# Performance work log

Hardware: AMD Instinct MI355X
Metric: run time of the kernel (lower is better)

Reference implementation:

```python
import jax, jax.numpy as jnp
import numpy as np
from jax import lax
import math

B, C, H, W = 8, 512, 24, 24
L = H * W
D_STATE = 16
D_INNER = 2 * C
DT_RANK = C // 16
K = 4
SCALE = 1.0 / math.sqrt(C)


def layer_norm(x, g, b, eps=1e-5):
    m = x.mean(-1, keepdims=True)
    v = ((x - m) ** 2).mean(-1, keepdims=True)
    return (x - m) * lax.rsqrt(v + eps) * g + b


def selective_scan(u, delta, A, Bm, Cm, Ds):
    # u, delta: (B,K,d,L); Bm, Cm: (B,K,N,L); A: (K,d,N); Ds: (K,d)
    us = jnp.moveaxis(u, -1, 0)      # (L,B,K,d)
    dts = jnp.moveaxis(delta, -1, 0)
    Bs = jnp.moveaxis(Bm, -1, 0)     # (L,B,K,N)
    Cs = jnp.moveaxis(Cm, -1, 0)

    def step(h, inp):
        u_t, dt_t, B_t, C_t = inp
        dA = jnp.exp(dt_t[..., None] * A)                      # (B,K,d,N)
        dBu = (dt_t * u_t)[..., None] * B_t[:, :, None, :]     # (B,K,d,N)
        h = dA * h + dBu
        y = jnp.einsum('bkdn,bkn->bkd', h, C_t)
        return h, y

    h0 = jnp.zeros(u.shape[:3] + (A.shape[-1],), u.dtype)
    _, ys = lax.scan(step, h0, (us, dts, Bs, Cs))
    y = jnp.moveaxis(ys, 0, -1)                                # (B,K,d,L)
    return y + Ds[None, :, :, None] * u


def ss2d(x, in_proj_w, dwconv_w, dwconv_b, x_proj_w, dt_proj_w, dt_proj_b,
         A_logs, Ds, out_norm_g, out_norm_b, out_proj_w):
    # x: (B,H,W,C) channel-last
    xz = x @ in_proj_w.T                                       # (B,H,W,2*d_inner)
    xi, z = jnp.split(xz, 2, axis=-1)
    xc = xi.transpose(0, 3, 1, 2)                              # (B,d_inner,H,W)
    xc = lax.conv_general_dilated(xc, dwconv_w, (1, 1), 'SAME',
                                  feature_group_count=D_INNER,
                                  dimension_numbers=('NCHW', 'OIHW', 'NCHW'))
    xc = jax.nn.silu(xc + dwconv_b[None, :, None, None])
    x_hw = xc.reshape(B, D_INNER, L)
    x_wh = xc.transpose(0, 1, 3, 2).reshape(B, D_INNER, L)
    xs = jnp.stack([x_hw, x_wh, x_hw[..., ::-1], x_wh[..., ::-1]], axis=1)  # (B,4,d,L)
    x_dbl = jnp.einsum('bkdl,kcd->bkcl', xs, x_proj_w)
    dt, Bm, Cm = jnp.split(x_dbl, [DT_RANK, DT_RANK + D_STATE], axis=2)
    delta = jax.nn.softplus(jnp.einsum('bkrl,kdr->bkdl', dt, dt_proj_w)
                            + dt_proj_b[None, :, :, None])
    A = -jnp.exp(A_logs)
    ys = selective_scan(xs, delta, A, Bm, Cm, Ds)              # (B,4,d,L)
    y_wh = ys[:, 1].reshape(B, D_INNER, W, H).transpose(0, 1, 3, 2).reshape(B, D_INNER, L)
    y_whr = ys[:, 3, :, ::-1].reshape(B, D_INNER, W, H).transpose(0, 1, 3, 2).reshape(B, D_INNER, L)
    y = ys[:, 0] + ys[:, 2, :, ::-1] + y_wh + y_whr
    y = y.reshape(B, D_INNER, H, W).transpose(0, 2, 3, 1)      # (B,H,W,d_inner)
    y = layer_norm(y, out_norm_g, out_norm_b)
    y = y * jax.nn.silu(z)
    return y @ out_proj_w.T                                    # (B,H,W,C)


def setup_inputs():
    key = jax.random.key(0)
    ks = jax.random.split(key, 10)
    n = lambda k, sh, s=0.02: jax.random.normal(k, sh, dtype=jnp.float32) * s
    return {
        'x5': jax.random.normal(ks[0], (B, C, H, W), dtype=jnp.float32),
        'conv_w': n(ks[1], (C, C)),
        'conv_b': jnp.zeros((C,), jnp.float32),
        'ln1_g': jnp.ones((C,), jnp.float32),
        'ln1_b': jnp.zeros((C,), jnp.float32),
        'in_proj_w': n(ks[2], (2 * D_INNER, C)),
        'dwconv_w': n(ks[3], (D_INNER, 1, 3, 3), 0.1),
        'dwconv_b': jnp.zeros((D_INNER,), jnp.float32),
        'x_proj_w': n(ks[4], (K, DT_RANK + 2 * D_STATE, D_INNER)),
        'dt_proj_w': n(ks[5], (K, D_INNER, DT_RANK), 0.1),
        'dt_proj_b': n(ks[6], (K, D_INNER), 0.1),
        'A_logs': jnp.tile(jnp.log(jnp.arange(1, D_STATE + 1, dtype=jnp.float32))[None, None, :],
                           (K, D_INNER, 1)),
        'Ds': jnp.ones((K, D_INNER), jnp.float32),
        'out_norm_g': jnp.ones((D_INNER,), jnp.float32),
        'out_norm_b': jnp.zeros((D_INNER,), jnp.float32),
        'out_proj_w': n(ks[7], (C, D_INNER)),
    }


def reference(x5, conv_w, conv_b, ln1_g, ln1_b, in_proj_w, dwconv_w, dwconv_b,
              x_proj_w, dt_proj_w, dt_proj_b, A_logs, Ds, out_norm_g, out_norm_b,
              out_proj_w):
    # 1x1 conv + residual
    x5 = jnp.einsum('bchw,oc->bohw', x5, conv_w) + conv_b[None, :, None, None] + x5
    x0 = x5.transpose(0, 2, 3, 1)                              # (B,H,W,C)
    # VSSBlock: x + SS2D(LN(x)); called twice on same input with same weights -> identical
    x00 = x0 + ss2d(layer_norm(x0, ln1_g, ln1_b), in_proj_w, dwconv_w, dwconv_b,
                    x_proj_w, dt_proj_w, dt_proj_b, A_logs, Ds,
                    out_norm_g, out_norm_b, out_proj_w)
    xq = x00.transpose(0, 3, 1, 2).reshape(B, C, L)            # (B,C,L)
    xq_flat = xq.transpose(0, 2, 1).reshape(B * L, C)          # (B*L, C)
    xk_flat = xq.transpose(1, 0, 2).reshape(C, B * L)          # (C, B*L)
    xw = (xq_flat @ xk_flat) * SCALE                           # (B*L, B*L)
    xw = xw.reshape(B * L, B, L).max(-1).mean(-1).reshape(B, L)
    xw = jax.nn.softmax(xw, axis=-1)
    norm0 = x5 / jnp.maximum(jnp.linalg.norm(x5, axis=1, keepdims=True), 1e-12)
    xw = xw[:, None, :]                                        # (B,1,L)
    xw_max = xw.max(-1, keepdims=True)
    mask = (xw == xw_max).astype(x5.dtype).reshape(B, 1, H, W)  # winner-take-all
    seeds = (norm0 * mask).sum((2, 3))                         # (B,C)
    # correlation (eval branch: relu), seeds act as 1x1 conv weights
    cor = jax.nn.relu(jnp.einsum('bchw,oc->bohw', norm0, seeds)).mean(1).reshape(B, L)
    mn = cor.min(1, keepdims=True)
    mx = cor.max(1, keepdims=True)
    cormap = ((cor - mn) / (mx - mn + 1e-12)).reshape(B, 1, H, W)
    x51 = x5 * cormap
    proto1 = x51.mean((0, 2, 3), keepdims=True)                # (1,C,1,1)
    return (x5, proto1, x5 * proto1 + x51, mask)
```

## Files before the change

kernel.cpp:

```cpp
#include <hip/hip_runtime.h>
#include <math.h>

#define NB 8
#define NC 512
#define NH 24
#define NW 24
#define NL 576
#define ND 1024
#define NBL 4608
#define NCH 8
#define CL 72

typedef __attribute__((ext_vector_type(8))) short bf16x8;
typedef __attribute__((ext_vector_type(4))) float f32x4;
typedef __attribute__((ext_vector_type(2))) float f32x2;

__device__ __forceinline__ unsigned enc_f(float f){
    unsigned u = __float_as_uint(f);
    return (u & 0x80000000u) ? ~u : (u | 0x80000000u);
}
__device__ __forceinline__ float dec_f(unsigned e){
    return (e & 0x80000000u) ? __uint_as_float(e ^ 0x80000000u) : __uint_as_float(~e);
}

__device__ __forceinline__ int scan_idx(int t, int k){
    int t2 = (k >= 2) ? (NL - 1 - t) : t;
    return (k & 1) ? ((t2 % NH) * NW + t2 / NH) : t2;
}

__device__ __forceinline__ float softplus_f(float x){
    return fmaxf(x, 0.f) + __logf(1.f + __expf(-fabsf(x)));
}
__device__ __forceinline__ float silu_f(float x){
    return x / (1.f + __expf(-x));
}

__device__ __forceinline__ void split_bf(float v, unsigned short &h, unsigned short &l){
    unsigned u = __float_as_uint(v);
    unsigned hr = (u + 0x7fffu + ((u>>16)&1u)) >> 16;
    h = (unsigned short)hr;
    float hf = __uint_as_float(hr << 16);
    unsigned u2 = __float_as_uint(v - hf);
    l = (unsigned short)((u2 + 0x7fffu + ((u2>>16)&1u)) >> 16);
}

__global__ void k_transpose_in(const float* __restrict__ x5, float* __restrict__ x5t,
                               unsigned short* __restrict__ x5tB){
    __shared__ float t[32][33];
    const int b = blockIdx.z;
    const int c0 = blockIdx.x*32, l0 = blockIdx.y*32;
    const int tx = threadIdx.x & 31, ty = threadIdx.x >> 5;
    #pragma unroll
    for (int i=ty; i<32; i+=8)
        t[i][tx] = x5[((size_t)b*NC + c0 + i)*NL + l0 + tx];
    __syncthreads();
    #pragma unroll
    for (int i=ty; i<32; i+=8){
        float v = t[tx][i];
        x5t[((size_t)b*NL + l0 + i)*NC + c0 + tx] = v;
        unsigned short hh, ll; split_bf(v, hh, ll);
        size_t rb = ((size_t)b*NL + l0 + i)*1536 + c0 + tx;
        x5tB[rb] = hh; x5tB[rb+512] = ll; x5tB[rb+1024] = hh;
    }
}

template<int FORM>
__global__ void k_split(const float* __restrict__ in, unsigned short* __restrict__ oA,
                        unsigned short* __restrict__ oB, int K, int total4){
    int t = blockIdx.x*256 + threadIdx.x;
    if (t >= total4) return;
    int kq = K >> 2;
    int r = t / kq; int k4 = (t - r*kq) << 2;
    float4 v = *(const float4*)(in + (size_t)r*K + k4);
    float vv[4] = {v.x, v.y, v.z, v.w};
    unsigned short h[4], lo[4];
    #pragma unroll
    for (int i=0;i<4;i++) split_bf(vv[i], h[i], lo[i]);
    unsigned hp0 = h[0] | ((unsigned)h[1]<<16), hp1 = h[2] | ((unsigned)h[3]<<16);
    unsigned lp0 = lo[0] | ((unsigned)lo[1]<<16), lp1 = lo[2] | ((unsigned)lo[3]<<16);
    size_t base = (size_t)r*3*K + k4;
    if (FORM == 0 || FORM == 2){
        unsigned* p0 = (unsigned*)(oA + base);
        unsigned* p1 = (unsigned*)(oA + base + K);
        unsigned* p2 = (unsigned*)(oA + base + 2*K);
        p0[0]=hp0; p0[1]=hp1;  p1[0]=hp0; p1[1]=hp1;  p2[0]=lp0; p2[1]=lp1;
    }
    if (FORM == 1 || FORM == 2){
        unsigned short* o = (FORM==2) ? oB : oA;
        unsigned* p0 = (unsigned*)(o + base);
        unsigned* p1 = (unsigned*)(o + base + K);
        unsigned* p2 = (unsigned*)(o + base + 2*K);
        p0[0]=hp0; p0[1]=hp1;  p1[0]=lp0; p1[1]=lp1;  p2[0]=hp0; p2[1]=hp1;
    }
}

template<int MODE>
__launch_bounds__(256)
__global__ void mfma_nt(const unsigned short* __restrict__ A, const unsigned short* __restrict__ Bm,
                        const float* __restrict__ R0, const float* __restrict__ R1,
                        float* __restrict__ out0, float* __restrict__ out1,
                        unsigned* __restrict__ mbuf, int K3)
{
    int bi, bj;
    if (MODE == 4){
        int rem = blockIdx.x, len = 36; bi = 0;
        while (rem >= len){ rem -= len; len--; bi++; }
        bj = bi + rem;
    } else { bi = blockIdx.x; bj = blockIdx.y; }
    const int m0 = bi*128, n0 = bj*128;
    __shared__ __align__(16) unsigned short As[128*32];
    __shared__ __align__(16) unsigned short Bs[128*32];
    const int tid = threadIdx.x;
    const int w = tid >> 6, l = tid & 63;
    const int mw = (w>>1)*64, nw = (w&1)*64;
    const int fr = l & 15, fq = l >> 4;

    f32x4 acc[4][4];
    #pragma unroll
    for (int i=0;i<4;i++)
        #pragma unroll
        for (int j=0;j<4;j++)
            #pragma unroll
            for (int c=0;c<4;c++) acc[i][j][c] = 0.f;

    const int c0 = tid, c1 = tid + 256;
    const int r0 = c0 >> 2, o0 = (c0 & 3) * 8;
    const int r1 = c1 >> 2, o1 = (c1 & 3) * 8;
    const unsigned short* pA0 = A  + (size_t)(m0 + r0)*K3 + o0;
    const unsigned short* pA1 = A  + (size_t)(m0 + r1)*K3 + o1;
    const unsigned short* pB0 = Bm + (size_t)(n0 + r0)*K3 + o0;
    const unsigned short* pB1 = Bm + (size_t)(n0 + r1)*K3 + o1;

    float4 a0 = *(const float4*)(pA0);
    float4 a1 = *(const float4*)(pA1);
    float4 b0 = *(const float4*)(pB0);
    float4 b1 = *(const float4*)(pB1);

    for (int k0 = 0; k0 < K3; k0 += 32){
        __syncthreads();
        *(float4*)&As[c0*8] = a0;
        *(float4*)&As[c1*8] = a1;
        *(float4*)&Bs[c0*8] = b0;
        *(float4*)&Bs[c1*8] = b1;
        __syncthreads();
        if (k0 + 32 < K3){
            a0 = *(const float4*)(pA0 + k0 + 32);
            a1 = *(const float4*)(pA1 + k0 + 32);
            b0 = *(const float4*)(pB0 + k0 + 32);
            b1 = *(const float4*)(pB1 + k0 + 32);
        }
        bf16x8 af[4], bf[4];
        #pragma unroll
        for (int i=0;i<4;i++){
            af[i] = *(const bf16x8*)&As[(mw + i*16 + fr)*32 + fq*8];
            bf[i] = *(const bf16x8*)&Bs[(nw + i*16 + fr)*32 + fq*8];
        }
        #pragma unroll
        for (int i=0;i<4;i++)
            #pragma unroll
            for (int j=0;j<4;j++)
                acc[i][j] = __builtin_amdgcn_mfma_f32_16x16x32_bf16(af[i], bf[j], acc[i][j], 0, 0, 0);
    }

    if (MODE == 4){
        const int b2c = (n0 + nw) / NL;
        #pragma unroll
        for (int mi=0; mi<4; mi++){
            #pragma unroll
            for (int i=0;i<4;i++){
                float v = fmaxf(fmaxf(acc[mi][0][i], acc[mi][1][i]),
                                fmaxf(acc[mi][2][i], acc[mi][3][i]));
                v = fmaxf(v, __shfl_xor(v, 1));
                v = fmaxf(v, __shfl_xor(v, 2));
                v = fmaxf(v, __shfl_xor(v, 4));
                v = fmaxf(v, __shfl_xor(v, 8));
                if (fr == 0)
                    atomicMax(&mbuf[(size_t)(m0 + mw + mi*16 + fq*4 + i)*NB + b2c], enc_f(v));
            }
        }
        const int b2r = (m0 + mw) / NL;
        #pragma unroll
        for (int ni=0; ni<4; ni++){
            float cm = -3.4e38f;
            #pragma unroll
            for (int mi=0; mi<4; mi++)
                #pragma unroll
                for (int i=0;i<4;i++) cm = fmaxf(cm, acc[mi][ni][i]);
            cm = fmaxf(cm, __shfl_xor(cm, 16));
            cm = fmaxf(cm, __shfl_xor(cm, 32));
            if (fq == 0)
                atomicMax(&mbuf[(size_t)(n0 + nw + ni*16 + fr)*NB + b2r], enc_f(cm));
        }
        return;
    }

    #pragma unroll
    for (int mi=0; mi<4; mi++){
        const int m = m0 + mw + mi*16 + fq*4;
        #pragma unroll
        for (int ni=0; ni<4; ni++){
            const int n = n0 + nw + ni*16 + fr;
            f32x4 a = acc[mi][ni];
            if (MODE == 0){
                float4 cb = *(const float4*)(R0 + m);
                float4 rs = *(const float4*)(R1 + (size_t)n*NC + m);
                float4 ov = make_float4(a[0]+cb.x+rs.x, a[1]+cb.y+rs.y, a[2]+cb.z+rs.z, a[3]+cb.w+rs.w);
                *(float4*)(out0 + (size_t)n*NC + m) = ov;
            } else if (MODE == 1){
                float4 ov = make_float4(a[0], a[1], a[2], a[3]);
                if (m < ND) *(float4*)(out0 + (size_t)n*ND + m) = ov;
                else        *(float4*)(out1 + (size_t)n*ND + (m - ND)) = ov;
            } else {
                float4 rs = *(const float4*)(R1 + (size_t)n*NC + m);
                float4 ov = make_float4(a[0]+rs.x, a[1]+rs.y, a[2]+rs.z, a[3]+rs.w);
                *(float4*)(out0 + (size_t)n*NC + m) = ov;
            }
        }
    }
}

template<int MODE>
__launch_bounds__(256)
__global__ void gemm_nt(const float* __restrict__ A0, const float* __restrict__ B0,
                        const float* __restrict__ R,
                        float* __restrict__ out0, float* __restrict__ out1,
                        unsigned* __restrict__ mbuf, int K)
{
    __shared__ __align__(16) float As[16][68];
    __shared__ __align__(16) float Bs[16][68];
    const int tid = threadIdx.x;
    const int m0 = blockIdx.x * 64;
    const int n0 = blockIdx.y * 64;
    const float* A = A0;
    const float* B = B0;
    int kdir = 0;
    if (MODE == 2) {
        const int bk = blockIdx.z;
        kdir = bk & 3; const int bb = bk >> 2;
        A = A0 + (size_t)kdir * 64 * 1024;
        B = B0 + (size_t)bb * NL * 1024;
    }
    const int lrow = tid >> 2;
    const int lk4  = (tid & 3) << 2;
    int brow = n0 + lrow;
    if (MODE == 2) brow = scan_idx(brow, kdir);
    const float* aptr = A + (size_t)(m0 + lrow) * K + lk4;
    const float* bptr = B + (size_t)brow * K + lk4;

    float acc[4][4];
    #pragma unroll
    for (int i=0;i<4;i++){
        #pragma unroll
        for (int j=0;j<4;j++) acc[i][j]=0.f;
    }
    const int tx = tid & 15, ty = tid >> 4;

    for (int k0 = 0; k0 < K; k0 += 16) {
        float4 av = *(const float4*)(aptr + k0);
        float4 bv = *(const float4*)(bptr + k0);
        __syncthreads();
        As[lk4+0][lrow]=av.x; As[lk4+1][lrow]=av.y; As[lk4+2][lrow]=av.z; As[lk4+3][lrow]=av.w;
        Bs[lk4+0][lrow]=bv.x; Bs[lk4+1][lrow]=bv.y; Bs[lk4+2][lrow]=bv.z; Bs[lk4+3][lrow]=bv.w;
        __syncthreads();
        #pragma unroll
        for (int kk=0;kk<16;kk++){
            float4 a = *(const float4*)&As[kk][ty<<2];
            float4 b = *(const float4*)&Bs[kk][tx<<2];
            acc[0][0] = fmaf(a.x,b.x,acc[0][0]); acc[0][1] = fmaf(a.x,b.y,acc[0][1]);
            acc[0][2] = fmaf(a.x,b.z,acc[0][2]); acc[0][3] = fmaf(a.x,b.w,acc[0][3]);
            acc[1][0] = fmaf(a.y,b.x,acc[1][0]); acc[1][1] = fmaf(a.y,b.y,acc[1][1]);
            acc[1][2] = fmaf(a.y,b.z,acc[1][2]); acc[1][3] = fmaf(a.y,b.w,acc[1][3]);
            acc[2][0] = fmaf(a.z,b.x,acc[2][0]); acc[2][1] = fmaf(a.z,b.y,acc[2][1]);
            acc[2][2] = fmaf(a.z,b.z,acc[2][2]); acc[2][3] = fmaf(a.z,b.w,acc[2][3]);
            acc[3][0] = fmaf(a.w,b.x,acc[3][0]); acc[3][1] = fmaf(a.w,b.y,acc[3][1]);
            acc[3][2] = fmaf(a.w,b.z,acc[3][2]); acc[3][3] = fmaf(a.w,b.w,acc[3][3]);
        }
    }

    #pragma unroll
    for (int j=0;j<4;j++){
        const int n  = n0 + (tx<<2) + j;
        const int mm = m0 + (ty<<2);
        float4 v = make_float4(acc[0][j], acc[1][j], acc[2][j], acc[3][j]);
        if (MODE == 2){
            *(float4*)(out0 + ((size_t)blockIdx.z*NL + n)*64 + mm) = v;
        }
    }
}

__global__ void k_ln512b(const float* __restrict__ x, const float* __restrict__ g,
                         const float* __restrict__ bb, unsigned short* __restrict__ outB){
    int n = blockIdx.x; int tid = threadIdx.x;
    const float* row = x + (size_t)n*NC;
    float v0 = row[tid], v1 = row[tid+256];
    __shared__ float s1[256], s2[256];
    s1[tid] = v0+v1; s2[tid] = v0*v0 + v1*v1;
    __syncthreads();
    for (int s=128;s>0;s>>=1){ if (tid<s){ s1[tid]+=s1[tid+s]; s2[tid]+=s2[tid+s]; } __syncthreads(); }
    float mean = s1[0]*(1.f/NC);
    float var  = fmaxf(s2[0]*(1.f/NC) - mean*mean, 0.f);
    float rs   = rsqrtf(var + 1e-5f);
    float r0 = (v0-mean)*rs*g[tid]     + bb[tid];
    float r1 = (v1-mean)*rs*g[tid+256] + bb[tid+256];
    unsigned short h0,l0,h1,l1; split_bf(r0,h0,l0); split_bf(r1,h1,l1);
    size_t base = (size_t)n*1536;
    outB[base+tid]     =h0; outB[base+512+tid]     =l0; outB[base+1024+tid]     =h0;
    outB[base+tid+256] =h1; outB[base+512+tid+256] =l1; outB[base+1024+tid+256] =h1;
}

__global__ void k_dwconv(const float* __restrict__ xi, const float* __restrict__ w,
                         const float* __restrict__ bias, float* __restrict__ xcl){
    int d = blockIdx.x*256 + threadIdx.x;
    int h = blockIdx.y; int b = blockIdx.z;
    float W[9];
    #pragma unroll
    for (int i=0;i<9;i++) W[i] = w[d*9+i];
    float bs = bias[d];
    const size_t rb = ((size_t)b*NL)*ND + d;
    const bool hm = h > 0, hp = h < NH-1;
    float p0=0.f,p1=0.f,p2=0.f;
    float c0 = hm ? xi[rb + (size_t)((h-1)*NW)*ND] : 0.f;
    float c1 = xi[rb + (size_t)(h*NW)*ND];
    float c2 = hp ? xi[rb + (size_t)((h+1)*NW)*ND] : 0.f;
    for (int wc=0; wc<NW; wc++){
        float n0,n1,n2;
        if (wc < NW-1){
            n0 = hm ? xi[rb + (size_t)((h-1)*NW+wc+1)*ND] : 0.f;
            n1 = xi[rb + (size_t)(h*NW+wc+1)*ND];
            n2 = hp ? xi[rb + (size_t)((h+1)*NW+wc+1)*ND] : 0.f;
        } else { n0=0.f;n1=0.f;n2=0.f; }
        float acc = bs;
        acc = fmaf(W[0],p0, fmaf(W[1],c0, fmaf(W[2],n0, acc)));
        acc = fmaf(W[3],p1, fmaf(W[4],c1, fmaf(W[5],n1, acc)));
        acc = fmaf(W[6],p2, fmaf(W[7],c2, fmaf(W[8],n2, acc)));
        xcl[rb + (size_t)(h*NW+wc)*ND] = silu_f(acc);
        p0=c0;p1=c1;p2=c2; c0=n0;c1=n1;c2=n2;
    }
}

#define DA_POWERS2 \
    float e2=e1*e1; float e3=e2*e1; float e4=e2*e2; \
    float e6=e4*e2; float e7=e4*e3; float e8=e4*e4; float e12=e8*e4; \
    f32x2 dA2[8]; \
    dA2[0]=(f32x2){e1,e2};       dA2[1]=(f32x2){e3,e4}; \
    dA2[2]=(f32x2){e4*e1,e6};    dA2[3]=(f32x2){e7,e8}; \
    dA2[4]=(f32x2){e8*e1,e8*e2}; dA2[5]=(f32x2){e8*e3,e12}; \
    dA2[6]=(f32x2){e12*e1,e12*e2}; dA2[7]=(f32x2){e12*e3,e8*e8};

#define DOTP_F4(rq4, dtb, out) { \
    f32x2 sA={0.f,0.f}, sB={0.f,0.f}; \
    _Pragma("unroll") \
    for (int i_=0;i_<8;i_++){ \
        float4 qq = rq4[i_]; \
        f32x2 lo; lo.x=qq.x; lo.y=qq.y; \
        f32x2 hi; hi.x=qq.z; hi.y=qq.w; \
        if (i_ & 1){ sB += lo*wdt2[2*i_]; sB += hi*wdt2[2*i_+1]; } \
        else       { sA += lo*wdt2[2*i_]; sA += hi*wdt2[2*i_+1]; } \
    } \
    out = (sA.x+sA.y)+(sB.x+sB.y)+dtb; }

__launch_bounds__(128)
__global__ void k_scan_p1(const float* __restrict__ xcl, const float* __restrict__ xdbl,
                          const float* __restrict__ dtw, const float* __restrict__ dtb,
                          const float* __restrict__ alogs,
                          float* __restrict__ hfin, float* __restrict__ prodA){
    const int d = blockIdx.x*128 + threadIdx.x;
    const int chunk = blockIdx.y;
    const int bk = blockIdx.z;
    const int k = bk & 3, b = bk >> 2;
    const int kd = k*ND + d;
    f32x2 wdt2[16];
    {
        const float4* p = (const float4*)(dtw + (size_t)kd*32);
        #pragma unroll
        for (int i=0;i<8;i++){
            float4 v=p[i];
            wdt2[2*i]   = (f32x2){v.x, v.y};
            wdt2[2*i+1] = (f32x2){v.z, v.w};
        }
    }
    float An[16]; bool ladder = true;
    {
        const float4* p = (const float4*)(alogs + (size_t)kd*16);
        #pragma unroll
        for (int i=0;i<4;i++){
            float4 v=p[i];
            An[4*i]=-__expf(v.x); An[4*i+1]=-__expf(v.y); An[4*i+2]=-__expf(v.z); An[4*i+3]=-__expf(v.w);
        }
        #pragma unroll
        for (int n=0;n<16;n++) ladder = ladder && (fabsf(An[n] + (float)(n+1)) < 1e-3f*(n+1));
    }
    const float dtbias = dtb[kd];
    __shared__ __align__(16) float rows[CL*64];
    {
        const float4* src = (const float4*)(xdbl + ((size_t)bk*NL + chunk*CL)*64);
        for (int i = threadIdx.x; i < CL*16; i += 128) ((float4*)rows)[i] = src[i];
    }
    __syncthreads();
    if (ladder){
        f32x2 h2[8], pA2[8];
        #pragma unroll
        for (int n=0;n<8;n++){ h2[n]=(f32x2){0.f,0.f}; pA2[n]=(f32x2){1.f,1.f}; }
        float u = xcl[((size_t)b*NL + scan_idx(chunk*CL, k))*ND + d];
        for (int t=0;t<CL;t++){
            const float4* rq4 = (const float4*)(rows + t*64);
            float dr; DOTP_F4(rq4, dtbias, dr);
            float u_cur = u;
            if (t+1 < CL) u = xcl[((size_t)b*NL + scan_idx(chunk*CL+t+1, k))*ND + d];
            float sp = softplus_f(dr);
            float du = sp * u_cur;
            float e1 = __expf(-sp);
            DA_POWERS2
            float4 qB[4];
            #pragma unroll
            for (int i=0;i<4;i++) qB[i] = rq4[8+i];
            f32x2 Bv[8];
            #pragma unroll
            for (int i=0;i<4;i++){
                Bv[2*i].x=qB[i].x; Bv[2*i].y=qB[i].y;
                Bv[2*i+1].x=qB[i].z; Bv[2*i+1].y=qB[i].w;
            }
            f32x2 du2 = (f32x2){du, du};
            #pragma unroll
            for (int n=0;n<8;n++){
                pA2[n] *= dA2[n];
                h2[n] = dA2[n]*h2[n] + du2*Bv[n];
            }
        }
        size_t base = (size_t)(bk*NCH + chunk)*16*1024 + d;
        #pragma unroll
        for (int n=0;n<8;n++){
            hfin[base + (2*n)*1024]   = h2[n].x;  hfin[base + (2*n+1)*1024] = h2[n].y;
            prodA[base + (2*n)*1024]  = pA2[n].x; prodA[base + (2*n+1)*1024]= pA2[n].y;
        }
    } else {
        float h[16], pA[16];
        #pragma unroll
        for (int n=0;n<16;n++){ h[n]=0.f; pA[n]=1.f; }
        for (int t=0;t<CL;t++){
            const float4* rq4 = (const float4*)(rows + t*64);
            float dr; DOTP_F4(rq4, dtbias, dr);
            float sp = softplus_f(dr);
            int idx = scan_idx(chunk*CL + t, k);
            float u  = xcl[((size_t)b*NL + idx)*ND + d];
            float du = sp * u;
            const float* row = rows + t*64;
            #pragma unroll
            for (int n=0;n<16;n++){
                float dA = __expf(sp * An[n]);
                pA[n] *= dA;
                h[n] = fmaf(dA, h[n], du*row[32+n]);
            }
        }
        size_t base = (size_t)(bk*NCH + chunk)*16*1024 + d;
        #pragma unroll
        for (int n=0;n<16;n++){ hfin[base + n*1024] = h[n]; prodA[base + n*1024] = pA[n]; }
    }
}

__global__ void k_scan_mid(float* __restrict__ hfin, const float* __restrict__ prodA){
    int id = blockIdx.x*256 + threadIdx.x;
    int d = id & 1023, nn = (id >> 10) & 15, bk = id >> 14;
    float h = 0.f;
    for (int j=0;j<NCH;j++){
        size_t idx = (size_t)((bk*NCH + j)*16 + nn)*1024 + d;
        float hf = hfin[idx], pa = prodA[idx];
        hfin[idx] = h;
        h = fmaf(pa, h, hf);
    }
}

__launch_bounds__(128)
__global__ void k_scan_p2(const float* __restrict__ xcl, const float* __restrict__ xdbl,
                          const float* __restrict__ dtw, const float* __restrict__ dtb,
                          const float* __restrict__ alogs,
                          const float* __restrict__ hfin, float* __restrict__ yacc){
    const int d = blockIdx.x*128 + threadIdx.x;
    const int chunk = blockIdx.y;
    const int bk = blockIdx.z;
    const int k = bk & 3, b = bk >> 2;
    const int kd = k*ND + d;
    f32x2 wdt2[16];
    {
        const float4* p = (const float4*)(dtw + (size_t)kd*32);
        #pragma unroll
        for (int i=0;i<8;i++){
            float4 v=p[i];
            wdt2[2*i]   = (f32x2){v.x, v.y};
            wdt2[2*i+1] = (f32x2){v.z, v.w};
        }
    }
    float An[16]; bool ladder = true;
    {
        const float4* p = (const float4*)(alogs + (size_t)kd*16);
        #pragma unroll
        for (int i=0;i<4;i++){
            float4 v=p[i];
            An[4*i]=-__expf(v.x); An[4*i+1]=-__expf(v.y); An[4*i+2]=-__expf(v.z); An[4*i+3]=-__expf(v.w);
        }
        #pragma unroll
        for (int n=0;n<16;n++) ladder = ladder && (fabsf(An[n] + (float)(n+1)) < 1e-3f*(n+1));
    }
    const float dtbias = dtb[kd];
    __shared__ __align__(16) float rows[CL*64];
    {
        const float4* src = (const float4*)(xdbl + ((size_t)bk*NL + chunk*CL)*64);
        for (int i = threadIdx.x; i < CL*16; i += 128) ((float4*)rows)[i] = src[i];
    }
    __syncthreads();
    if (ladder){
        f32x2 h2[8];
        {
            size_t base = (size_t)(bk*NCH + chunk)*16*1024 + d;
            #pragma unroll
            for (int n=0;n<8;n++)
                h2[n] = (f32x2){hfin[base + (2*n)*1024], hfin[base + (2*n+1)*1024]};
        }
        int idx = scan_idx(chunk*CL, k);
        float u = xcl[((size_t)b*NL + idx)*ND + d];
        for (int t=0;t<CL;t++){
            const float4* rq4 = (const float4*)(rows + t*64);
            float dr; DOTP_F4(rq4, dtbias, dr);
            float u_cur = u; int idx_cur = idx;
            if (t+1 < CL){
                idx = scan_idx(chunk*CL+t+1, k);
                u = xcl[((size_t)b*NL + idx)*ND + d];
            }
            float sp = softplus_f(dr);
            float du = sp * u_cur;
            float e1 = __expf(-sp);
            DA_POWERS2
            float4 qB[4], qC[4];
            #pragma unroll
            for (int i=0;i<4;i++){ qB[i] = rq4[8+i]; qC[i] = rq4[12+i]; }
            f32x2 Bv[8], Cv[8];
            #pragma unroll
            for (int i=0;i<4;i++){
                Bv[2*i].x=qB[i].x; Bv[2*i].y=qB[i].y;
                Bv[2*i+1].x=qB[i].z; Bv[2*i+1].y=qB[i].w;
                Cv[2*i].x=qC[i].x; Cv[2*i].y=qC[i].y;
                Cv[2*i+1].x=qC[i].z; Cv[2*i+1].y=qC[i].w;
            }
            f32x2 du2 = (f32x2){du, du};
            f32x2 y2 = (f32x2){0.f, 0.f};
            #pragma unroll
            for (int n=0;n<8;n++){
                h2[n] = dA2[n]*h2[n] + du2*Bv[n];
                y2 += h2[n]*Cv[n];
            }
            atomicAdd(&yacc[((size_t)b*NL + idx_cur)*ND + d], y2.x + y2.y);
        }
    } else {
        float h[16];
        {
            size_t base = (size_t)(bk*NCH + chunk)*16*1024 + d;
            #pragma unroll
            for (int n=0;n<16;n++) h[n] = hfin[base + n*1024];
        }
        for (int t=0;t<CL;t++){
            const float4* rq4 = (const float4*)(rows + t*64);
            float dr; DOTP_F4(rq4, dtbias, dr);
            float sp = softplus_f(dr);
            int idx = scan_idx(chunk*CL + t, k);
            size_t base = ((size_t)b*NL + idx)*ND + d;
            float u  = xcl[base];
            float du = sp * u;
            const float* row = rows + t*64;
            float y = 0.f;
            #pragma unroll
            for (int n=0;n<16;n++){
                float dA = __expf(sp * An[n]);
                h[n] = fmaf(dA, h[n], du*row[32+n]);
                y = fmaf(h[n], row[48+n], y);
            }
            atomicAdd(&yacc[base], y);
        }
    }
}

__global__ void k_combine(const float* __restrict__ y, const float* __restrict__ xcl,
                          const float* __restrict__ Ds,
                          const float* __restrict__ g, const float* __restrict__ bb,
                          const float* __restrict__ z, unsigned short* __restrict__ zB){
    int n = blockIdx.x;
    size_t base = (size_t)n*ND;
    int tid = threadIdx.x;
    float v[4]; float sum=0.f, sq=0.f;
    #pragma unroll
    for (int j=0;j<4;j++){
        int d = tid + 256*j;
        float ds = Ds[d] + Ds[ND+d] + Ds[2*ND+d] + Ds[3*ND+d];
        float val = y[base+d] + ds*xcl[base+d];
        v[j]=val; sum+=val; sq+=val*val;
    }
    __shared__ float s1[256], s2[256];
    s1[tid]=sum; s2[tid]=sq; __syncthreads();
    for (int st=128;st>0;st>>=1){ if(tid<st){ s1[tid]+=s1[tid+st]; s2[tid]+=s2[tid+st]; } __syncthreads(); }
    float mean = s1[0]*(1.f/ND);
    float var  = fmaxf(s2[0]*(1.f/ND) - mean*mean, 0.f);
    float rs   = rsqrtf(var + 1e-5f);
    size_t zb = (size_t)n*3072;
    #pragma unroll
    for (int j=0;j<4;j++){
        int d = tid + 256*j;
        float ln = (v[j]-mean)*rs*g[d] + bb[d];
        float res = ln * silu_f(z[base+d]);
        unsigned short hh,ll; split_bf(res,hh,ll);
        zB[zb + d] = hh; zB[zb + 1024 + d] = ll; zB[zb + 2048 + d] = hh;
    }
}

__global__ void k_mask2(const unsigned* __restrict__ M, float* __restrict__ maskf,
                        int* __restrict__ hitcnt, int* __restrict__ hitidx){
    int b = blockIdx.x; int tid = threadIdx.x;
    __shared__ int lcnt;
    if (tid == 0) lcnt = 0;
    __syncthreads();
    float loc[9];
    float m = -3.4e38f;
    #pragma unroll
    for (int j=0;j<9;j++){
        int l = tid + j*64;
        float s = 0.f;
        #pragma unroll
        for (int b2=0;b2<NB;b2++) s += dec_f(M[(size_t)(b*NL+l)*NB + b2]);
        loc[j] = s; m = fmaxf(m, s);
    }
    #pragma unroll
    for (int s=32;s>0;s>>=1) m = fmaxf(m, __shfl_xor(m, s));
    #pragma unroll
    for (int j=0;j<9;j++){
        int l = tid + j*64;
        bool hit = (loc[j] == m);
        maskf[b*NL + l] = hit ? 1.f : 0.f;
        if (hit){
            int pos = atomicAdd(&lcnt, 1);
            hitidx[b*NL + pos] = l;
        }
    }
    __syncthreads();
    if (tid == 0) hitcnt[b] = lcnt;
}

__global__ void k_norm0(const float* __restrict__ x5r, float* __restrict__ norm0){
    int n = blockIdx.x; int tid = threadIdx.x;
    float v0 = x5r[(size_t)n*NC+tid], v1 = x5r[(size_t)n*NC+tid+256];
    __shared__ float s1[256];
    s1[tid] = v0*v0 + v1*v1; __syncthreads();
    for (int st=128;st>0;st>>=1){ if(tid<st) s1[tid]+=s1[tid+st]; __syncthreads(); }
    float inv = 1.f / fmaxf(sqrtf(s1[0]), 1e-12f);
    norm0[(size_t)n*NC+tid]     = v0*inv;
    norm0[(size_t)n*NC+tid+256] = v1*inv;
}

__global__ void k_seeds(const float* __restrict__ norm0, const int* __restrict__ hitcnt,
                        const int* __restrict__ hitidx, float* __restrict__ seeds){
    int b = blockIdx.x; int c = threadIdx.x;
    int cnt = hitcnt[b];
    float acc = 0.f;
    for (int i=0;i<cnt;i++){
        int l = hitidx[b*NL + i];
        acc += norm0[((size_t)b*NL+l)*NC + c];
    }
    seeds[b*NC + c] = acc;
}

__global__ void k_cor(const float* __restrict__ norm0, const float* __restrict__ seeds,
                      float* __restrict__ cor){
    int n = blockIdx.x; int tid = threadIdx.x;
    int o = tid >> 6, lane = tid & 63;
    float acc = 0.f;
    #pragma unroll
    for (int i=0;i<8;i++){
        int c = lane + 64*i;
        acc += norm0[(size_t)n*NC + c] * seeds[o*NC + c];
    }
    #pragma unroll
    for (int s=32;s>0;s>>=1) acc += __shfl_xor(acc, s);
    __shared__ float sr[8];
    if (lane == 0) sr[o] = fmaxf(acc, 0.f);
    __syncthreads();
    if (tid == 0){
        float r = 0.f;
        #pragma unroll
        for (int o2=0;o2<8;o2++) r += sr[o2];
        cor[n] = r * (1.f/8.f);
    }
}

__global__ void k_cormap(const float* __restrict__ cor, float* __restrict__ cmap){
    int b = blockIdx.x, tid = threadIdx.x;
    float mn = 1e30f, mx = -1e30f;
    for (int i=tid;i<NL;i+=64){ float v=cor[b*NL+i]; mn=fminf(mn,v); mx=fmaxf(mx,v); }
    __shared__ float sn[64], sx[64];
    sn[tid]=mn; sx[tid]=mx; __syncthreads();
    for (int st=32;st>0;st>>=1){ if(tid<st){ sn[tid]=fminf(sn[tid],sn[tid+st]); sx[tid]=fmaxf(sx[tid],sx[tid+st]); } __syncthreads(); }
    float MN=sn[0], MX=sx[0];
    float inv = 1.f/(MX-MN+1e-12f);
    for (int i=tid;i<NL;i+=64) cmap[b*NL+i] = (cor[b*NL+i]-MN)*inv;
}

__global__ void k_proto(const float* __restrict__ x5r, const float* __restrict__ cmap,
                        float* __restrict__ pacc){
    int c = threadIdx.x;
    int chunk = blockIdx.x;
    float acc = 0.f;
    for (int i=0;i<64;i++){
        int n = chunk*64 + i;
        acc += x5r[(size_t)n*NC + c] * cmap[n];
    }
    atomicAdd(&pacc[c], acc);
}

__global__ void k_final_t(const float* __restrict__ x5r, const float* __restrict__ cmap,
                          const float* __restrict__ pacc, float* __restrict__ out){
    __shared__ float t[32][33];
    const int b = blockIdx.z;
    const int c0 = blockIdx.x*32, l0 = blockIdx.y*32;
    const int tx = threadIdx.x & 31, ty = threadIdx.x >> 5;
    #pragma unroll
    for (int i=ty; i<32; i+=8)
        t[i][tx] = x5r[((size_t)b*NL + l0 + i)*NC + c0 + tx];
    __syncthreads();
    #pragma unroll
    for (int i=ty; i<32; i+=8){
        float v = t[tx][i];
        int c = c0 + i, l = l0 + tx;
        size_t o = ((size_t)b*NC + c)*NL + l;
        out[o] = v;
        out[2359808 + o] = v*(pacc[c]*(1.f/(float)NBL) + cmap[b*NL + l]);
    }
}

__global__ void k_final_s(const float* __restrict__ pacc, const float* __restrict__ maskf,
                          float* __restrict__ out){
    int id = blockIdx.x*256 + threadIdx.x;
    if (id < 512) out[2359296 + id] = pacc[id]*(1.f/(float)NBL);
    int j = id - 512;
    if (j >= 0 && j < NBL) out[2359808 + 2359296 + j] = maskf[j];
}

extern "C" void kernel_launch(void* const* d_in, const int* in_sizes, int n_in,
                              void* d_out, int out_size, void* d_ws, size_t ws_size,
                              hipStream_t stream) {
    const float* x5        = (const float*)d_in[0];
    const float* conv_w    = (const float*)d_in[1];
    const float* conv_b    = (const float*)d_in[2];
    const float* ln1_g     = (const float*)d_in[3];
    const float* ln1_b     = (const float*)d_in[4];
    const float* in_proj_w = (const float*)d_in[5];
    const float* dwconv_w  = (const float*)d_in[6];
    const float* dwconv_b  = (const float*)d_in[7];
    const float* x_proj_w  = (const float*)d_in[8];
    const float* dt_proj_w = (const float*)d_in[9];
    const float* dt_proj_b = (const float*)d_in[10];
    const float* A_logs    = (const float*)d_in[11];
    const float* Ds        = (const float*)d_in[12];
    const float* out_norm_g= (const float*)d_in[13];
    const float* out_norm_b= (const float*)d_in[14];
    const float* out_proj_w= (const float*)d_in[15];

    float* ws = (float*)d_ws;
    const size_t O_X5R  = 0;
    const size_t O_XLN  = 2359296;
    const size_t O_XI   = 4718592;
    const size_t O_Z    = 9437184;
    const size_t O_XCL  = 14155776;
    const size_t O_XDBL = 18874368;
    const size_t O_HF   = 20054016;
    const size_t O_PA   = 24248320;
    const size_t O_MBUF = 28442624;
    const size_t O_MASK = 28484096;
    const size_t O_COR  = 28488704;
    const size_t O_CMAP = 28493312;
    const size_t O_SEED = 28497920;
    const size_t O_PACC = 28502016;
    const size_t O_HITC = 28502528;
    const size_t O_HITI = 28502544;

    float* x5r  = ws + O_X5R;
    float* xqf  = ws + O_XLN;
    float* xi   = ws + O_XI;
    float* yacc = ws + O_XI;
    unsigned short* wAo = (unsigned short*)(ws + O_XI);
    float* z    = ws + O_Z;
    float* xcl  = ws + O_XCL;
    unsigned short* wAi = (unsigned short*)(ws + O_XCL);
    float* nrm0 = ws + O_XCL;
    float* xdbl = ws + O_XDBL;
    float* x5t  = ws + O_HF;
    float* hfin = ws + O_HF;
    unsigned short* xlnB = (unsigned short*)(ws + O_HF);
    unsigned short* zB   = (unsigned short*)(ws + O_HF);
    unsigned short* xqfA = (unsigned short*)(ws + O_HF);
    float* prodA = ws + O_PA;
    unsigned short* x5tB = (unsigned short*)(ws + O_PA);
    unsigned short* wAc  = (unsigned short*)(ws + O_PA) + 7077888;
    unsigned short* xqfB = (unsigned short*)(ws + O_PA);
    unsigned* mbuf = (unsigned*)(ws + O_MBUF);
    float* maskf= ws + O_MASK;
    float* cor  = ws + O_COR;
    float* cmap = ws + O_CMAP;
    float* seeds= ws + O_SEED;
    float* pacc = ws + O_PACC;
    int* hitcnt = (int*)(ws + O_HITC);
    int* hitidx = (int*)(ws + O_HITI);

    (void)hipMemsetAsync(mbuf, 0, 36864*sizeof(unsigned), stream);
    (void)hipMemsetAsync(pacc, 0, 512*sizeof(float), stream);

    k_transpose_in<<<dim3(16,18,8), 256, 0, stream>>>(x5, x5t, x5tB);
    k_split<0><<<256, 256, 0, stream>>>(conv_w, wAc, nullptr, 512, 65536);
    mfma_nt<0><<<dim3(4,36), 256, 0, stream>>>(wAc, x5tB, conv_b, x5t, x5r, nullptr, nullptr, 1536);
    k_ln512b<<<NBL, 256, 0, stream>>>(x5r, ln1_g, ln1_b, xlnB);
    k_split<0><<<1024, 256, 0, stream>>>(in_proj_w, wAi, nullptr, 512, 262144);
    mfma_nt<1><<<dim3(16,36), 256, 0, stream>>>(wAi, xlnB, nullptr, nullptr, xi, z, nullptr, 1536);
    k_dwconv<<<dim3(4,NH,NB), 256, 0, stream>>>(xi, dwconv_w, dwconv_b, xcl);
    (void)hipMemsetAsync(yacc, 0, (size_t)4718592*sizeof(float), stream);
    gemm_nt<2><<<dim3(1,9,32), 256, 0, stream>>>(x_proj_w, xcl, nullptr, xdbl, nullptr, nullptr, 1024);
    k_scan_p1<<<dim3(8,NCH,32), 128, 0, stream>>>(xcl, xdbl, dt_proj_w, dt_proj_b, A_logs, hfin, prodA);
    k_scan_mid<<<2048, 256, 0, stream>>>(hfin, prodA);
    k_scan_p2<<<dim3(8,NCH,32), 128, 0, stream>>>(xcl, xdbl, dt_proj_w, dt_proj_b, A_logs, hfin, yacc);
    k_combine<<<NBL, 256, 0, stream>>>(yacc, xcl, Ds, out_norm_g, out_norm_b, z, zB);
    k_split<0><<<512, 256, 0, stream>>>(out_proj_w, wAo, nullptr, 1024, 131072);
    mfma_nt<3><<<dim3(4,36), 256, 0, stream>>>(wAo, zB, nullptr, x5r, xqf, nullptr, nullptr, 3072);
    k_split<2><<<2304, 256, 0, stream>>>(xqf, xqfA, xqfB, 512, 589824);
    mfma_nt<4><<<666, 256, 0, stream>>>(xqfA, xqfB, nullptr, nullptr, nullptr, nullptr, mbuf, 1536);
    k_mask2<<<NB, 64, 0, stream>>>(mbuf, maskf, hitcnt, hitidx);
    k_norm0<<<NBL, 256, 0, stream>>>(x5r, nrm0);
    k_seeds<<<NB, 512, 0, stream>>>(nrm0, hitcnt, hitidx, seeds);
    k_cor<<<NBL, 512, 0, stream>>>(nrm0, seeds, cor);
    k_cormap<<<NB, 64, 0, stream>>>(cor, cmap);
    k_proto<<<72, 512, 0, stream>>>(x5r, cmap, pacc);
    k_final_t<<<dim3(16,18,8), 256, 0, stream>>>(x5r, cmap, pacc, (float*)d_out);
    k_final_s<<<20, 256, 0, stream>>>(pacc, maskf, (float*)d_out);
}
```

Baseline: 607.2 us.

## Pad GEMM LDS tiles, vectorize depthwise conv, prefetch scan dt rows

Pads the shared-memory A/B tiles in the MFMA GEMM to a 40-element row stride so the 16-byte fragment reads land in fewer conflicting LDS banks. Rewrites the depthwise conv so each thread handles two adjacent channels with float2 loads and stores, halving the thread count per block. Software-prefetches the next timestep's dt-row data into registers in the scan kernels so LDS reads overlap the dot product. The padding uses more LDS per block and the prefetch raises register pressure in the scan kernels.

```diff
diff --git a/kernel.cpp b/kernel.cpp
--- a/kernel.cpp
+++ b/kernel.cpp
@@ -10,6 +10,7 @@
 #define NBL 4608
 #define NCH 8
 #define CL 72
+#define LDP 40
 
 typedef __attribute__((ext_vector_type(8))) short bf16x8;
 typedef __attribute__((ext_vector_type(4))) float f32x4;
@@ -108,8 +109,8 @@
         bj = bi + rem;
     } else { bi = blockIdx.x; bj = blockIdx.y; }
     const int m0 = bi*128, n0 = bj*128;
-    __shared__ __align__(16) unsigned short As[128*32];
-    __shared__ __align__(16) unsigned short Bs[128*32];
+    __shared__ __align__(16) unsigned short As[128*LDP];
+    __shared__ __align__(16) unsigned short Bs[128*LDP];
     const int tid = threadIdx.x;
     const int w = tid >> 6, l = tid & 63;
     const int mw = (w>>1)*64, nw = (w&1)*64;
@@ -138,10 +139,10 @@
 
     for (int k0 = 0; k0 < K3; k0 += 32){
         __syncthreads();
-        *(float4*)&As[c0*8] = a0;
-        *(float4*)&As[c1*8] = a1;
-        *(float4*)&Bs[c0*8] = b0;
-        *(float4*)&Bs[c1*8] = b1;
+        *(float4*)&As[r0*LDP + o0] = a0;
+        *(float4*)&As[r1*LDP + o1] = a1;
+        *(float4*)&Bs[r0*LDP + o0] = b0;
+        *(float4*)&Bs[r1*LDP + o1] = b1;
         __syncthreads();
         if (k0 + 32 < K3){
             a0 = *(const float4*)(pA0 + k0 + 32);
@@ -152,8 +153,8 @@
         bf16x8 af[4], bf[4];
         #pragma unroll
         for (int i=0;i<4;i++){
-            af[i] = *(const bf16x8*)&As[(mw + i*16 + fr)*32 + fq*8];
-            bf[i] = *(const bf16x8*)&Bs[(nw + i*16 + fr)*32 + fq*8];
+            af[i] = *(const bf16x8*)&As[(mw + i*16 + fr)*LDP + fq*8];
+            bf[i] = *(const bf16x8*)&Bs[(nw + i*16 + fr)*LDP + fq*8];
         }
         #pragma unroll
         for (int i=0;i<4;i++)
@@ -310,30 +311,33 @@
 
 __global__ void k_dwconv(const float* __restrict__ xi, const float* __restrict__ w,
                          const float* __restrict__ bias, float* __restrict__ xcl){
-    int d = blockIdx.x*256 + threadIdx.x;
+    int dp = blockIdx.x*128 + threadIdx.x;
+    int d0 = dp*2;
     int h = blockIdx.y; int b = blockIdx.z;
-    float W[9];
-    #pragma unroll
-    for (int i=0;i<9;i++) W[i] = w[d*9+i];
-    float bs = bias[d];
-    const size_t rb = ((size_t)b*NL)*ND + d;
+    f32x2 W[9];
+    #pragma unroll
+    for (int i=0;i<9;i++){ W[i].x = w[d0*9+i]; W[i].y = w[(d0+1)*9+i]; }
+    f32x2 bs; bs.x = bias[d0]; bs.y = bias[d0+1];
+    const size_t rb = ((size_t)b*NL)*ND + d0;
     const bool hm = h > 0, hp = h < NH-1;
-    float p0=0.f,p1=0.f,p2=0.f;
-    float c0 = hm ? xi[rb + (size_t)((h-1)*NW)*ND] : 0.f;
-    float c1 = xi[rb + (size_t)(h*NW)*ND];
-    float c2 = hp ? xi[rb + (size_t)((h+1)*NW)*ND] : 0.f;
+    f32x2 zr = (f32x2){0.f,0.f};
+    f32x2 p0=zr,p1=zr,p2=zr;
+    f32x2 c0 = hm ? *(const f32x2*)&xi[rb + (size_t)((h-1)*NW)*ND] : zr;
+    f32x2 c1 = *(const f32x2*)&xi[rb + (size_t)(h*NW)*ND];
+    f32x2 c2 = hp ? *(const f32x2*)&xi[rb + (size_t)((h+1)*NW)*ND] : zr;
     for (int wc=0; wc<NW; wc++){
-        float n0,n1,n2;
+        f32x2 n0,n1,n2;
         if (wc < NW-1){
-            n0 = hm ? xi[rb + (size_t)((h-1)*NW+wc+1)*ND] : 0.f;
-            n1 = xi[rb + (size_t)(h*NW+wc+1)*ND];
-            n2 = hp ? xi[rb + (size_t)((h+1)*NW+wc+1)*ND] : 0.f;
-        } else { n0=0.f;n1=0.f;n2=0.f; }
-        float acc = bs;
-        acc = fmaf(W[0],p0, fmaf(W[1],c0, fmaf(W[2],n0, acc)));
-        acc = fmaf(W[3],p1, fmaf(W[4],c1, fmaf(W[5],n1, acc)));
-        acc = fmaf(W[6],p2, fmaf(W[7],c2, fmaf(W[8],n2, acc)));
-        xcl[rb + (size_t)(h*NW+wc)*ND] = silu_f(acc);
+            n0 = hm ? *(const f32x2*)&xi[rb + (size_t)((h-1)*NW+wc+1)*ND] : zr;
+            n1 = *(const f32x2*)&xi[rb + (size_t)(h*NW+wc+1)*ND];
+            n2 = hp ? *(const f32x2*)&xi[rb + (size_t)((h+1)*NW+wc+1)*ND] : zr;
+        } else { n0=zr;n1=zr;n2=zr; }
+        f32x2 acc = bs;
+        acc += W[0]*p0 + W[1]*c0 + W[2]*n0;
+        acc += W[3]*p1 + W[4]*c1 + W[5]*n1;
+        acc += W[6]*p2 + W[7]*c2 + W[8]*n2;
+        f32x2 s; s.x = silu_f(acc.x); s.y = silu_f(acc.y);
+        *(f32x2*)&xcl[rb + (size_t)(h*NW+wc)*ND] = s;
         p0=c0;p1=c1;p2=c2; c0=n0;c1=n1;c2=n2;
     }
 }
@@ -347,11 +351,11 @@
     dA2[4]=(f32x2){e8*e1,e8*e2}; dA2[5]=(f32x2){e8*e3,e12}; \
     dA2[6]=(f32x2){e12*e1,e12*e2}; dA2[7]=(f32x2){e12*e3,e8*e8};
 
-#define DOTP_F4(rq4, dtb, out) { \
+#define DOTR(dtc, dtb, out) { \
     f32x2 sA={0.f,0.f}, sB={0.f,0.f}; \
     _Pragma("unroll") \
     for (int i_=0;i_<8;i_++){ \
-        float4 qq = rq4[i_]; \
+        float4 qq = dtc[i_]; \
         f32x2 lo; lo.x=qq.x; lo.y=qq.y; \
         f32x2 hi; hi.x=qq.z; hi.y=qq.w; \
         if (i_ & 1){ sB += lo*wdt2[2*i_]; sB += hi*wdt2[2*i_+1]; } \
@@ -402,9 +406,21 @@
         #pragma unroll
         for (int n=0;n<8;n++){ h2[n]=(f32x2){0.f,0.f}; pA2[n]=(f32x2){1.f,1.f}; }
         float u = xcl[((size_t)b*NL + scan_idx(chunk*CL, k))*ND + d];
+        float4 dtc[8];
+        {
+            const float4* r0p = (const float4*)rows;
+            #pragma unroll
+            for (int i=0;i<8;i++) dtc[i] = r0p[i];
+        }
         for (int t=0;t<CL;t++){
             const float4* rq4 = (const float4*)(rows + t*64);
-            float dr; DOTP_F4(rq4, dtbias, dr);
+            float4 dtn[8];
+            if (t+1 < CL){
+                const float4* rn = (const float4*)(rows + (t+1)*64);
+                #pragma unroll
+                for (int i=0;i<8;i++) dtn[i] = rn[i];
+            }
+            float dr; DOTR(dtc, dtbias, dr);
             float u_cur = u;
             if (t+1 < CL) u = xcl[((size_t)b*NL + scan_idx(chunk*CL+t+1, k))*ND + d];
             float sp = softplus_f(dr);
@@ -426,6 +442,8 @@
                 pA2[n] *= dA2[n];
                 h2[n] = dA2[n]*h2[n] + du2*Bv[n];
             }
+            #pragma unroll
+            for (int i=0;i<8;i++) dtc[i] = dtn[i];
         }
         size_t base = (size_t)(bk*NCH + chunk)*16*1024 + d;
         #pragma unroll
@@ -439,7 +457,10 @@
         for (int n=0;n<16;n++){ h[n]=0.f; pA[n]=1.f; }
         for (int t=0;t<CL;t++){
             const float4* rq4 = (const float4*)(rows + t*64);
-            float dr; DOTP_F4(rq4, dtbias, dr);
+            float4 dtc[8];
+            #pragma unroll
+            for (int i=0;i<8;i++) dtc[i] = rq4[i];
+            float dr; DOTR(dtc, dtbias, dr);
             float sp = softplus_f(dr);
             int idx = scan_idx(chunk*CL + t, k);
             float u  = xcl[((size_t)b*NL + idx)*ND + d];
@@ -518,9 +539,21 @@
         }
         int idx = scan_idx(chunk*CL, k);
         float u = xcl[((size_t)b*NL + idx)*ND + d];
+        float4 dtc[8];
+        {
+            const float4* r0p = (const float4*)rows;
+            #pragma unroll
+            for (int i=0;i<8;i++) dtc[i] = r0p[i];
+        }
         for (int t=0;t<CL;t++){
             const float4* rq4 = (const float4*)(rows + t*64);
-            float dr; DOTP_F4(rq4, dtbias, dr);
+            float4 dtn[8];
+            if (t+1 < CL){
+                const float4* rn = (const float4*)(rows + (t+1)*64);
+                #pragma unroll
+                for (int i=0;i<8;i++) dtn[i] = rn[i];
+            }
+            float dr; DOTR(dtc, dtbias, dr);
             float u_cur = u; int idx_cur = idx;
             if (t+1 < CL){
                 idx = scan_idx(chunk*CL+t+1, k);
@@ -549,6 +582,8 @@
                 y2 += h2[n]*Cv[n];
             }
             atomicAdd(&yacc[((size_t)b*NL + idx_cur)*ND + d], y2.x + y2.y);
+            #pragma unroll
+            for (int i=0;i<8;i++) dtc[i] = dtn[i];
         }
     } else {
         float h[16];
@@ -559,7 +594,10 @@
         }
         for (int t=0;t<CL;t++){
             const float4* rq4 = (const float4*)(rows + t*64);
-            float dr; DOTP_F4(rq4, dtbias, dr);
+            float4 dtc[8];
+            #pragma unroll
+            for (int i=0;i<8;i++) dtc[i] = rq4[i];
+            float dr; DOTR(dtc, dtbias, dr);
             float sp = softplus_f(dr);
             int idx = scan_idx(chunk*CL + t, k);
             size_t base = ((size_t)b*NL + idx)*ND + d;
@@ -815,7 +853,7 @@
     k_ln512b<<<NBL, 256, 0, stream>>>(x5r, ln1_g, ln1_b, xlnB);
     k_split<0><<<1024, 256, 0, stream>>>(in_proj_w, wAi, nullptr, 512, 262144);
     mfma_nt<1><<<dim3(16,36), 256, 0, stream>>>(wAi, xlnB, nullptr, nullptr, xi, z, nullptr, 1536);
-    k_dwconv<<<dim3(4,NH,NB), 256, 0, stream>>>(xi, dwconv_w, dwconv_b, xcl);
+    k_dwconv<<<dim3(4,NH,NB), 128, 0, stream>>>(xi, dwconv_w, dwconv_b, xcl);
     (void)hipMemsetAsync(yacc, 0, (size_t)4718592*sizeof(float), stream);
     gemm_nt<2><<<dim3(1,9,32), 256, 0, stream>>>(x_proj_w, xcl, nullptr, xdbl, nullptr, nullptr, 1024);
     k_scan_p1<<<dim3(8,NCH,32), 128, 0, stream>>>(xcl, xdbl, dt_proj_w, dt_proj_b, A_logs, hfin, prodA);
```

Result: slower. 638.3 us (+5.1%).
